# Optimization experiments

Measured on AMD Instinct MI355X. Metric: run time of the kernel, lower is better.

Reference implementation:

```python
import jax, jax.numpy as jnp
import numpy as np

NODE_DIM = 256
EDGE_DIM = 32
HIDDEN = 128
N_NODES = 100000
N_EDGES = 1000000


def setup_inputs() -> dict:
    key = jax.random.key(0)
    k_z, k_ei, k_ea, k_w1, k_b1, k_w2, k_b2 = jax.random.split(key, 7)
    in_dim = NODE_DIM * 2 + EDGE_DIM
    z = jax.random.normal(k_z, (N_NODES, NODE_DIM), dtype=jnp.float32)
    edge_label_index = jax.random.randint(k_ei, (2, N_EDGES), 0, N_NODES, dtype=jnp.int64)
    edge_attr = jax.random.normal(k_ea, (N_EDGES, EDGE_DIM), dtype=jnp.float32)
    # nn.Linear-style init: U(-1/sqrt(fan_in), 1/sqrt(fan_in))
    s1 = 1.0 / np.sqrt(in_dim)
    s2 = 1.0 / np.sqrt(HIDDEN)
    W1 = jax.random.uniform(k_w1, (in_dim, HIDDEN), jnp.float32, -s1, s1)
    b1 = jax.random.uniform(k_b1, (HIDDEN,), jnp.float32, -s1, s1)
    W2 = jax.random.uniform(k_w2, (HIDDEN, 1), jnp.float32, -s2, s2)
    b2 = jax.random.uniform(k_b2, (1,), jnp.float32, -s2, s2)
    return {"z": z, "edge_label_index": edge_label_index, "edge_attr": edge_attr,
            "W1": W1, "b1": b1, "W2": W2, "b2": b2}


def reference(z, edge_label_index, edge_attr, W1, b1, W2, b2):
    src = edge_label_index[0]
    dst = edge_label_index[1]
    # [E, 2*node_dim + edge_dim] concatenated edge features
    feat = jnp.concatenate([z[src], z[dst], edge_attr], axis=-1)
    h = jax.nn.relu(feat @ W1 + b1)          # [E, 128]
    out = h @ W2 + b2                        # [E, 1]
    return out.reshape(-1)                   # [E]
```

## Files before the change

kernel.cpp:

```cpp
#include <hip/hip_runtime.h>

typedef __attribute__((ext_vector_type(8))) short short8;
typedef __attribute__((ext_vector_type(8))) unsigned short ushort8;
typedef __attribute__((ext_vector_type(4))) unsigned short ushort4v;
typedef __attribute__((ext_vector_type(4))) float f32x4;

__device__ __forceinline__ unsigned short f2bf(float f) {
  unsigned int u = __float_as_uint(f);
  u += 0x7fffu + ((u >> 16) & 1u);
  return (unsigned short)(u >> 16);
}
__device__ __forceinline__ float bf2f(unsigned short u) {
  return __uint_as_float(((unsigned int)u) << 16);
}
__device__ __forceinline__ void gl_lds16(const void* g, void* l) {
  __builtin_amdgcn_global_load_lds(
      (const __attribute__((address_space(1))) unsigned int*)g,
      (__attribute__((address_space(3))) unsigned int*)l, 16, 0, 0);
}

__global__ void prep_weights(const float* __restrict__ W1,
                             unsigned short* __restrict__ W1T2,
                             unsigned short* __restrict__ W1cT) {
  int idx = blockIdx.x * 256 + threadIdx.x;
  if (idx < 65536) {
    int np = idx >> 8, k = idx & 255;
    W1T2[idx] = f2bf(W1[(size_t)(k + ((np >> 7) << 8)) * 128 + (np & 127)]);
  } else if (idx < 65536 + 4096) {
    int j = idx - 65536;
    int n = j >> 5, k = j & 31;
    W1cT[j] = f2bf(W1[(size_t)(512 + k) * 128 + n]);
  }
}

__global__ __launch_bounds__(256) void node_proj(
    const float* __restrict__ z, const unsigned short* __restrict__ W1T2,
    unsigned short* __restrict__ Ps, int NN) {
  __shared__ unsigned short As[2][128 * 32];
  __shared__ unsigned short Bs[2][128 * 32];
  const int tid = threadIdx.x, wid = tid >> 6, lane = tid & 63;
  const int wrow = wid >> 1, wcol = wid & 1;
  const int quad = lane >> 4, l15 = lane & 15;
  const int lrow = lane >> 2, lch = lane & 3;
  const int bm = blockIdx.x, half = blockIdx.y;

  const int r0 = 32 * wid + lrow, r1 = r0 + 16;
  const int m0 = min(bm * 128 + r0, NN - 1);
  const int m1 = min(bm * 128 + r1, NN - 1);
  const float* a0 = z + (size_t)m0 * 256;
  const float* a1 = z + (size_t)m1 * 256;

  f32x4 acc[4][4] = {};

  auto stage = [&](int ks, int b) {
#pragma unroll
    for (int j = 0; j < 2; ++j) {
      int nb = 2 * wid + j;
      const unsigned short* g =
          W1T2 + (size_t)(half * 128 + nb * 16 + lrow) * 256 + ks * 32 + lch * 8;
      gl_lds16(g, &Bs[b][nb * 512]);
    }
#pragma unroll
    for (int j = 0; j < 2; ++j) {
      const float* g = (j ? a1 : a0) + ks * 32 + lch * 8;
      f32x4 a = *(const f32x4*)g;
      f32x4 c = *(const f32x4*)(g + 4);
      ushort8 o;
      o[0]=f2bf(a[0]); o[1]=f2bf(a[1]); o[2]=f2bf(a[2]); o[3]=f2bf(a[3]);
      o[4]=f2bf(c[0]); o[5]=f2bf(c[1]); o[6]=f2bf(c[2]); o[7]=f2bf(c[3]);
      *(ushort8*)&As[b][(j ? r1 : r0) * 32 + lch * 8] = o;
    }
  };

  auto compute = [&](int b) {
    short8 af[4], bfv[4];
#pragma unroll
    for (int i = 0; i < 4; ++i) {
      af[i]  = *(const short8*)&As[b][(wrow * 64 + i * 16 + l15) * 32 + quad * 8];
      bfv[i] = *(const short8*)&Bs[b][(wcol * 64 + i * 16 + l15) * 32 + quad * 8];
    }
#pragma unroll
    for (int mi = 0; mi < 4; ++mi)
#pragma unroll
      for (int ni = 0; ni < 4; ++ni)
        acc[mi][ni] = __builtin_amdgcn_mfma_f32_16x16x32_bf16(af[mi], bfv[ni], acc[mi][ni], 0, 0, 0);
  };

  stage(0, 0);
#pragma unroll
  for (int s = 0; s < 8; ++s) {
    __syncthreads();
    if (s + 1 < 8) stage(s + 1, (s + 1) & 1);
    compute(s & 1);
  }

#pragma unroll
  for (int mi = 0; mi < 4; ++mi) {
#pragma unroll
    for (int r = 0; r < 4; ++r) {
      int row = wrow * 64 + mi * 16 + quad * 4 + r;
      int node = bm * 128 + row;
      if (node < NN) {
        ushort4v o;
#pragma unroll
        for (int ni = 0; ni < 4; ++ni) o[ni] = f2bf(acc[mi][ni][r]);
        *(ushort4v*)&Ps[(size_t)node * 256 + half * 128 + l15 * 8 + wcol * 4] = o;
      }
    }
  }
}

__global__ __launch_bounds__(256) void edge_pred(
    const int* __restrict__ eidx, const float* __restrict__ ea,
    const unsigned short* __restrict__ Ps, const unsigned short* __restrict__ W1cT,
    const float* __restrict__ b1, const float* __restrict__ W2,
    const float* __restrict__ b2, float* __restrict__ out, int E) {
  __shared__ unsigned short EaS[128 * 32];
  __shared__ unsigned short WcS[128 * 32];
  const int tid = threadIdx.x, wid = tid >> 6, lane = tid & 63;
  const int quad = lane >> 4, l15 = lane & 15;
  const int lrow = lane >> 2, lch = lane & 3;
  const int be = blockIdx.x * 128;

#pragma unroll
  for (int j = 0; j < 2; ++j) {
    int nb = 2 * wid + j;
    gl_lds16(W1cT + (size_t)(nb * 16 + lrow) * 32 + lch * 8, &WcS[nb * 512]);
  }

  {
    int e_loc = tid >> 1, part = tid & 1;
    size_t e_g = (size_t)min(be + e_loc, E - 1);
    const float* g = ea + e_g * 32 + part * 16;
    f32x4 a = *(const f32x4*)g;
    f32x4 b = *(const f32x4*)(g + 4);
    f32x4 c = *(const f32x4*)(g + 8);
    f32x4 d = *(const f32x4*)(g + 12);
    ushort8 o1, o2;
    o1[0]=f2bf(a[0]); o1[1]=f2bf(a[1]); o1[2]=f2bf(a[2]); o1[3]=f2bf(a[3]);
    o1[4]=f2bf(b[0]); o1[5]=f2bf(b[1]); o1[6]=f2bf(b[2]); o1[7]=f2bf(b[3]);
    o2[0]=f2bf(c[0]); o2[1]=f2bf(c[1]); o2[2]=f2bf(c[2]); o2[3]=f2bf(c[3]);
    o2[4]=f2bf(d[0]); o2[5]=f2bf(d[1]); o2[6]=f2bf(d[2]); o2[7]=f2bf(d[3]);
    *(ushort8*)&EaS[e_loc * 32 + part * 16] = o1;
    *(ushort8*)&EaS[e_loc * 32 + part * 16 + 8] = o2;
  }

  int srcn[8], dstn[8];
#pragma unroll
  for (int mi = 0; mi < 2; ++mi)
#pragma unroll
    for (int r = 0; r < 4; ++r) {
      int t = mi * 4 + r;
      int ec = min(be + wid * 32 + mi * 16 + quad * 4 + r, E - 1);
      srcn[t] = eidx[ec];
      dstn[t] = eidx[E + ec];
    }
  short8 p1[8], p2[8];
#pragma unroll
  for (int t = 0; t < 8; ++t) {
    p1[t] = *(const short8*)&Ps[(size_t)srcn[t] * 256 + l15 * 8];
    p2[t] = *(const short8*)&Ps[(size_t)dstn[t] * 256 + 128 + l15 * 8];
  }

  __syncthreads();

  short8 af[2], bfv[8];
#pragma unroll
  for (int mi = 0; mi < 2; ++mi)
    af[mi] = *(const short8*)&EaS[(wid * 32 + mi * 16 + l15) * 32 + quad * 8];
#pragma unroll
  for (int ni = 0; ni < 8; ++ni)
    bfv[ni] = *(const short8*)&WcS[(ni * 16 + l15) * 32 + quad * 8];

  f32x4 acc[2][8] = {};
#pragma unroll
  for (int mi = 0; mi < 2; ++mi)
#pragma unroll
    for (int ni = 0; ni < 8; ++ni)
      acc[mi][ni] = __builtin_amdgcn_mfma_f32_16x16x32_bf16(af[mi], bfv[ni], acc[mi][ni], 0, 0, 0);

  float b1v[8], w2v[8];
#pragma unroll
  for (int ni = 0; ni < 8; ++ni) {
    int c = ni * 16 + l15;
    b1v[ni] = b1[c];
    w2v[ni] = W2[c];
  }
  const float b2v = b2[0];

#pragma unroll
  for (int mi = 0; mi < 2; ++mi) {
#pragma unroll
    for (int r = 0; r < 4; ++r) {
      int t = mi * 4 + r;
      float p = 0.f;
#pragma unroll
      for (int ni = 0; ni < 8; ++ni) {
        float s = bf2f((unsigned short)p1[t][ni]) + bf2f((unsigned short)p2[t][ni]);
        float h = acc[mi][ni][r] + s + b1v[ni];
        h = fmaxf(h, 0.f);
        p = fmaf(h, w2v[ni], p);
      }
      p += __shfl_xor(p, 1);
      p += __shfl_xor(p, 2);
      p += __shfl_xor(p, 4);
      p += __shfl_xor(p, 8);
      int e = be + wid * 32 + mi * 16 + quad * 4 + r;
      if (l15 == 0 && e < E) out[e] = p + b2v;
    }
  }
}

extern "C" void kernel_launch(void* const* d_in, const int* in_sizes, int n_in,
                              void* d_out, int out_size, void* d_ws, size_t ws_size,
                              hipStream_t stream) {
  const float* z   = (const float*)d_in[0];
  const int*   eix = (const int*)d_in[1];
  const float* ea  = (const float*)d_in[2];
  const float* W1  = (const float*)d_in[3];
  const float* b1  = (const float*)d_in[4];
  const float* W2  = (const float*)d_in[5];
  const float* b2  = (const float*)d_in[6];
  float* out = (float*)d_out;

  const int E  = in_sizes[1] / 2;
  const int NN = in_sizes[0] / 256;

  unsigned short* wsp = (unsigned short*)d_ws;
  unsigned short* Ps   = wsp;
  unsigned short* W1T2 = wsp + (size_t)NN * 256;
  unsigned short* W1cT = W1T2 + 65536;

  prep_weights<<<273, 256, 0, stream>>>(W1, W1T2, W1cT);

  dim3 gp((NN + 127) / 128, 2);
  node_proj<<<gp, 256, 0, stream>>>(z, W1T2, Ps, NN);

  int ge = (E + 127) / 128;
  edge_pred<<<ge, 256, 0, stream>>>(eix, ea, Ps, W1cT, b1, W2, b2, out, E);
}
```

Baseline: 346.4 us.

## Widen node projection tile to all 256 outputs and pre-seed edge accumulators

node_proj now computes both output halves in one block (128x256 tile), so each z row is read and converted to bf16 once instead of twice, at the cost of more accumulator registers (launch bounds set to 2 blocks per CU) and a non-unrolled k-loop. edge_pred issues the index and edge_attr loads earlier to overlap their latency, and initializes the MFMA accumulators with the gathered src+dst projections instead of adding them afterwards. Occupancy hints are added to edge_pred as well.

Measured after the change: 349.2 us. Within noise of the previous version (+0.8%).

```diff
diff --git a/kernel.cpp b/kernel.cpp
--- a/kernel.cpp
+++ b/kernel.cpp
@@ -2,7 +2,6 @@
 
 typedef __attribute__((ext_vector_type(8))) short short8;
 typedef __attribute__((ext_vector_type(8))) unsigned short ushort8;
-typedef __attribute__((ext_vector_type(4))) unsigned short ushort4v;
 typedef __attribute__((ext_vector_type(4))) float f32x4;
 
 __device__ __forceinline__ unsigned short f2bf(float f) {
@@ -33,61 +32,64 @@
   }
 }
 
-__global__ __launch_bounds__(256) void node_proj(
+__global__ __launch_bounds__(256, 2) void node_proj(
     const float* __restrict__ z, const unsigned short* __restrict__ W1T2,
     unsigned short* __restrict__ Ps, int NN) {
   __shared__ unsigned short As[2][128 * 32];
-  __shared__ unsigned short Bs[2][128 * 32];
+  __shared__ unsigned short Bs[2][256 * 32];
   const int tid = threadIdx.x, wid = tid >> 6, lane = tid & 63;
   const int wrow = wid >> 1, wcol = wid & 1;
   const int quad = lane >> 4, l15 = lane & 15;
   const int lrow = lane >> 2, lch = lane & 3;
-  const int bm = blockIdx.x, half = blockIdx.y;
-
-  const int r0 = 32 * wid + lrow, r1 = r0 + 16;
-  const int m0 = min(bm * 128 + r0, NN - 1);
-  const int m1 = min(bm * 128 + r1, NN - 1);
-  const float* a0 = z + (size_t)m0 * 256;
-  const float* a1 = z + (size_t)m1 * 256;
-
-  f32x4 acc[4][4] = {};
-
-  auto stage = [&](int ks, int b) {
+  const int bm = blockIdx.x;
+
+  const float* zsrc[2];
+  int rr[2];
+#pragma unroll
+  for (int j = 0; j < 2; ++j) {
+    rr[j] = (2 * wid + j) * 16 + lrow;
+    int node = min(bm * 128 + rr[j], NN - 1);
+    zsrc[j] = z + (size_t)node * 256;
+  }
+
+  f32x4 acc[4][8] = {};
+
+  auto stage = [&](int ks, int bb) {
+#pragma unroll
+    for (int j = 0; j < 4; ++j) {
+      int nb = 4 * wid + j;
+      gl_lds16(W1T2 + (size_t)(nb * 16 + lrow) * 256 + ks * 32 + lch * 8,
+               &Bs[bb][nb * 512]);
+    }
 #pragma unroll
     for (int j = 0; j < 2; ++j) {
-      int nb = 2 * wid + j;
-      const unsigned short* g =
-          W1T2 + (size_t)(half * 128 + nb * 16 + lrow) * 256 + ks * 32 + lch * 8;
-      gl_lds16(g, &Bs[b][nb * 512]);
-    }
-#pragma unroll
-    for (int j = 0; j < 2; ++j) {
-      const float* g = (j ? a1 : a0) + ks * 32 + lch * 8;
+      const float* g = zsrc[j] + ks * 32 + lch * 8;
       f32x4 a = *(const f32x4*)g;
       f32x4 c = *(const f32x4*)(g + 4);
       ushort8 o;
       o[0]=f2bf(a[0]); o[1]=f2bf(a[1]); o[2]=f2bf(a[2]); o[3]=f2bf(a[3]);
       o[4]=f2bf(c[0]); o[5]=f2bf(c[1]); o[6]=f2bf(c[2]); o[7]=f2bf(c[3]);
-      *(ushort8*)&As[b][(j ? r1 : r0) * 32 + lch * 8] = o;
+      *(ushort8*)&As[bb][rr[j] * 32 + lch * 8] = o;
     }
   };
 
-  auto compute = [&](int b) {
-    short8 af[4], bfv[4];
-#pragma unroll
-    for (int i = 0; i < 4; ++i) {
-      af[i]  = *(const short8*)&As[b][(wrow * 64 + i * 16 + l15) * 32 + quad * 8];
-      bfv[i] = *(const short8*)&Bs[b][(wcol * 64 + i * 16 + l15) * 32 + quad * 8];
-    }
+  auto compute = [&](int bb) {
+    short8 af[4], bfv[8];
+#pragma unroll
+    for (int i = 0; i < 4; ++i)
+      af[i] = *(const short8*)&As[bb][(wrow * 64 + i * 16 + l15) * 32 + quad * 8];
+#pragma unroll
+    for (int i = 0; i < 8; ++i)
+      bfv[i] = *(const short8*)&Bs[bb][(wcol * 128 + i * 16 + l15) * 32 + quad * 8];
 #pragma unroll
     for (int mi = 0; mi < 4; ++mi)
 #pragma unroll
-      for (int ni = 0; ni < 4; ++ni)
+      for (int ni = 0; ni < 8; ++ni)
         acc[mi][ni] = __builtin_amdgcn_mfma_f32_16x16x32_bf16(af[mi], bfv[ni], acc[mi][ni], 0, 0, 0);
   };
 
   stage(0, 0);
-#pragma unroll
+#pragma unroll 1
   for (int s = 0; s < 8; ++s) {
     __syncthreads();
     if (s + 1 < 8) stage(s + 1, (s + 1) & 1);
@@ -101,16 +103,16 @@
       int row = wrow * 64 + mi * 16 + quad * 4 + r;
       int node = bm * 128 + row;
       if (node < NN) {
-        ushort4v o;
-#pragma unroll
-        for (int ni = 0; ni < 4; ++ni) o[ni] = f2bf(acc[mi][ni][r]);
-        *(ushort4v*)&Ps[(size_t)node * 256 + half * 128 + l15 * 8 + wcol * 4] = o;
+        ushort8 o;
+#pragma unroll
+        for (int ni = 0; ni < 8; ++ni) o[ni] = f2bf(acc[mi][ni][r]);
+        *(ushort8*)&Ps[(size_t)node * 256 + wcol * 128 + l15 * 8] = o;
       }
     }
   }
 }
 
-__global__ __launch_bounds__(256) void edge_pred(
+__global__ __launch_bounds__(256, 3) void edge_pred(
     const int* __restrict__ eidx, const float* __restrict__ ea,
     const unsigned short* __restrict__ Ps, const unsigned short* __restrict__ W1cT,
     const float* __restrict__ b1, const float* __restrict__ W2,
@@ -122,39 +124,27 @@
   const int lrow = lane >> 2, lch = lane & 3;
   const int be = blockIdx.x * 128;
 
+  int srcn[8], dstn[8];
+#pragma unroll
+  for (int t = 0; t < 8; ++t) {
+    int ec = min(be + wid * 32 + (t >> 2) * 16 + quad * 4 + (t & 3), E - 1);
+    srcn[t] = eidx[ec];
+    dstn[t] = eidx[E + ec];
+  }
+
+  const int e_loc = tid >> 1, part = tid & 1;
+  const float* gea = ea + (size_t)min(be + e_loc, E - 1) * 32 + part * 16;
+  f32x4 va = *(const f32x4*)gea;
+  f32x4 vb = *(const f32x4*)(gea + 4);
+  f32x4 vc = *(const f32x4*)(gea + 8);
+  f32x4 vd = *(const f32x4*)(gea + 12);
+
 #pragma unroll
   for (int j = 0; j < 2; ++j) {
     int nb = 2 * wid + j;
     gl_lds16(W1cT + (size_t)(nb * 16 + lrow) * 32 + lch * 8, &WcS[nb * 512]);
   }
 
-  {
-    int e_loc = tid >> 1, part = tid & 1;
-    size_t e_g = (size_t)min(be + e_loc, E - 1);
-    const float* g = ea + e_g * 32 + part * 16;
-    f32x4 a = *(const f32x4*)g;
-    f32x4 b = *(const f32x4*)(g + 4);
-    f32x4 c = *(const f32x4*)(g + 8);
-    f32x4 d = *(const f32x4*)(g + 12);
-    ushort8 o1, o2;
-    o1[0]=f2bf(a[0]); o1[1]=f2bf(a[1]); o1[2]=f2bf(a[2]); o1[3]=f2bf(a[3]);
-    o1[4]=f2bf(b[0]); o1[5]=f2bf(b[1]); o1[6]=f2bf(b[2]); o1[7]=f2bf(b[3]);
-    o2[0]=f2bf(c[0]); o2[1]=f2bf(c[1]); o2[2]=f2bf(c[2]); o2[3]=f2bf(c[3]);
-    o2[4]=f2bf(d[0]); o2[5]=f2bf(d[1]); o2[6]=f2bf(d[2]); o2[7]=f2bf(d[3]);
-    *(ushort8*)&EaS[e_loc * 32 + part * 16] = o1;
-    *(ushort8*)&EaS[e_loc * 32 + part * 16 + 8] = o2;
-  }
-
-  int srcn[8], dstn[8];
-#pragma unroll
-  for (int mi = 0; mi < 2; ++mi)
-#pragma unroll
-    for (int r = 0; r < 4; ++r) {
-      int t = mi * 4 + r;
-      int ec = min(be + wid * 32 + mi * 16 + quad * 4 + r, E - 1);
-      srcn[t] = eidx[ec];
-      dstn[t] = eidx[E + ec];
-    }
   short8 p1[8], p2[8];
 #pragma unroll
   for (int t = 0; t < 8; ++t) {
@@ -162,6 +152,27 @@
     p2[t] = *(const short8*)&Ps[(size_t)dstn[t] * 256 + 128 + l15 * 8];
   }
 
+  {
+    ushort8 o1, o2;
+    o1[0]=f2bf(va[0]); o1[1]=f2bf(va[1]); o1[2]=f2bf(va[2]); o1[3]=f2bf(va[3]);
+    o1[4]=f2bf(vb[0]); o1[5]=f2bf(vb[1]); o1[6]=f2bf(vb[2]); o1[7]=f2bf(vb[3]);
+    o2[0]=f2bf(vc[0]); o2[1]=f2bf(vc[1]); o2[2]=f2bf(vc[2]); o2[3]=f2bf(vc[3]);
+    o2[4]=f2bf(vd[0]); o2[5]=f2bf(vd[1]); o2[6]=f2bf(vd[2]); o2[7]=f2bf(vd[3]);
+    *(ushort8*)&EaS[e_loc * 32 + part * 16] = o1;
+    *(ushort8*)&EaS[e_loc * 32 + part * 16 + 8] = o2;
+  }
+
+  f32x4 acc[2][8];
+#pragma unroll
+  for (int mi = 0; mi < 2; ++mi)
+#pragma unroll
+    for (int r = 0; r < 4; ++r) {
+      int t = mi * 4 + r;
+#pragma unroll
+      for (int ni = 0; ni < 8; ++ni)
+        acc[mi][ni][r] = bf2f((unsigned short)p1[t][ni]) + bf2f((unsigned short)p2[t][ni]);
+    }
+
   __syncthreads();
 
   short8 af[2], bfv[8];
@@ -172,7 +183,6 @@
   for (int ni = 0; ni < 8; ++ni)
     bfv[ni] = *(const short8*)&WcS[(ni * 16 + l15) * 32 + quad * 8];
 
-  f32x4 acc[2][8] = {};
 #pragma unroll
   for (int mi = 0; mi < 2; ++mi)
 #pragma unroll
@@ -192,12 +202,10 @@
   for (int mi = 0; mi < 2; ++mi) {
 #pragma unroll
     for (int r = 0; r < 4; ++r) {
-      int t = mi * 4 + r;
       float p = 0.f;
 #pragma unroll
       for (int ni = 0; ni < 8; ++ni) {
-        float s = bf2f((unsigned short)p1[t][ni]) + bf2f((unsigned short)p2[t][ni]);
-        float h = acc[mi][ni][r] + s + b1v[ni];
+        float h = acc[mi][ni][r] + b1v[ni];
         h = fmaxf(h, 0.f);
         p = fmaf(h, w2v[ni], p);
       }
@@ -233,8 +241,8 @@
 
   prep_weights<<<273, 256, 0, stream>>>(W1, W1T2, W1cT);
 
-  dim3 gp((NN + 127) / 128, 2);
-  node_proj<<<gp, 256, 0, stream>>>(z, W1T2, Ps, NN);
+  int nbm = (NN + 127) / 128;
+  node_proj<<<nbm, 256, 0, stream>>>(z, W1T2, Ps, NN);
 
   int ge = (E + 127) / 128;
   edge_pred<<<ge, 256, 0, stream>>>(eix, ea, Ps, W1cT, b1, W2, b2, out, E);
```
